# Kernel tuning notes

Measured on AMD Instinct MI355X. Metric: run time of the kernel, lower is better.

## Reference

```python
import jax, jax.numpy as jnp
import numpy as np

EPS = 1e-5

def _layernorm(x, gamma, beta):
    # normalize over last (channel) axis, per point
    mu = jnp.mean(x, axis=-1, keepdims=True)
    var = jnp.mean(jnp.square(x - mu), axis=-1, keepdims=True)
    return (x - mu) * jax.lax.rsqrt(var + EPS) * gamma + beta

def setup_inputs() -> dict:
    key = jax.random.key(0)
    ks = jax.random.split(key, 12)
    B, N, C, F = 32, 4096, 3, 1024
    points = jax.random.normal(ks[0], (B, N, C), dtype=jnp.float32)
    mask = jax.random.randint(ks[1], (B, 1, N), 0, 2, dtype=jnp.int32)
    s = 0.05
    return {
        "points": points,
        "mask": mask,
        "w1": jax.random.normal(ks[2], (128, C), dtype=jnp.float32) * s,      # conv1 (no bias)
        "g1": jnp.ones((128,), jnp.float32),                                   # norm1 gamma
        "be1": jnp.zeros((128,), jnp.float32),                                 # norm1 beta
        "w2": jax.random.normal(ks[3], (256, 128), dtype=jnp.float32) * s,     # conv2
        "b2": jax.random.normal(ks[4], (256,), dtype=jnp.float32) * s,
        "w3": jax.random.normal(ks[5], (512, 512), dtype=jnp.float32) * s,     # conv3 (no bias)
        "g2": jnp.ones((512,), jnp.float32),                                   # norm2 gamma
        "be2": jnp.zeros((512,), jnp.float32),                                 # norm2 beta
        "w4": jax.random.normal(ks[6], (F, 512), dtype=jnp.float32) * s,       # conv4
        "b4": jax.random.normal(ks[7], (F,), dtype=jnp.float32) * s,
    }

def reference(points, mask, w1, g1, be1, w2, b2, w3, g2, be2, w4, b4):
    # points: [B, N, C]; mask: [B, 1, N]
    vis = (mask[:, 0, :] != 0).astype(points.dtype)[..., None]  # [B, N, 1]
    # conv1 (1x1, no bias) as point-wise matmul
    h0 = jnp.einsum('bnc,kc->bnk', points, w1)                  # [B, N, 128]
    # masked LayerNorm: LN is per-point over channels, so compute densely and zero invisible points
    h1 = _layernorm(h0, g1, be1) * vis
    h2 = jax.nn.relu(h1)
    h3 = jnp.einsum('bnk,ok->bno', h2, w2) + b2                 # [B, N, 256]
    gmax = jnp.max(h3, axis=1, keepdims=True)                   # [B, 1, 256]
    dist = jnp.concatenate([jnp.broadcast_to(gmax, h3.shape), h3], axis=-1)  # [B, N, 512]
    h4 = jnp.einsum('bno,po->bnp', dist, w3)                    # [B, N, 512]
    h5 = _layernorm(h4, g2, be2) * vis
    h6 = jax.nn.relu(h5)
    h7 = jnp.einsum('bnp,fp->bnf', h6, w4) + b4                 # [B, N, F]
    return jnp.max(h7, axis=1)                                  # [B, F]
```

## Files before the change

### kernel.cpp

```cpp
#include <hip/hip_runtime.h>
#include <stdint.h>

#define LN_EPS 1e-5f

static __device__ __forceinline__ unsigned short f2bf_bits(float f) {
  union { float f; unsigned u; } v; v.f = f;
  unsigned r = v.u + 0x7FFFu + ((v.u >> 16) & 1u);
  return (unsigned short)(r >> 16);
}
static __device__ __forceinline__ float bf2f(unsigned short h) {
  union { unsigned u; float f; } v; v.u = ((unsigned)h) << 16;
  return v.f;
}

typedef __bf16 bf16x8 __attribute__((ext_vector_type(8)));
typedef float floatx4 __attribute__((ext_vector_type(4)));

typedef __attribute__((address_space(1))) unsigned int* gas_ptr;
typedef __attribute__((address_space(3))) unsigned int* las_ptr;
static __device__ __forceinline__ void async_cp16(const void* g, void* l) {
  __builtin_amdgcn_global_load_lds((gas_ptr)g, (las_ptr)l, 16, 0, 0);
}

__global__ __launch_bounds__(256) void perm_kernel(
    const int* __restrict__ mask, int* __restrict__ newrow, int* __restrict__ cnt) {
  const int b = blockIdx.x, t = threadIdx.x;
  const int base = b * 4096 + t * 16;
  int v[16]; int s = 0;
#pragma unroll
  for (int i = 0; i < 16; ++i) { v[i] = (mask[base + i] != 0); s += v[i]; }
  const int lane = t & 63, wv = t >> 6;
  int scan = s;
  for (int o = 1; o < 64; o <<= 1) { int x = __shfl_up(scan, o); if (lane >= o) scan += x; }
  __shared__ int wsum[4], woff[4], stotal;
  if (lane == 63) wsum[wv] = scan;
  __syncthreads();
  if (t == 0) { int a = 0; for (int k = 0; k < 4; ++k) { woff[k] = a; a += wsum[k]; } stotal = a; cnt[b] = a; }
  __syncthreads();
  const int excl = scan - s + woff[wv];
  const int total = stotal;
  int run = 0;
#pragma unroll
  for (int i = 0; i < 16; ++i) {
    const int pos = t * 16 + i;
    const int visBefore = excl + run;
    newrow[b * 4096 + pos] = v[i] ? visBefore : total + (pos - visBefore);
    run += v[i];
  }
}

__global__ __launch_bounds__(256) void conv1_ln_kernel(
    const float* __restrict__ points,
    const float* __restrict__ w1, const float* __restrict__ g1,
    const float* __restrict__ be1, unsigned short* __restrict__ h2,
    const int* __restrict__ newrow, const int* __restrict__ cnt,
    const float* __restrict__ w2, const float* __restrict__ b2,
    const float* __restrict__ w3, const float* __restrict__ w4,
    unsigned short* __restrict__ w2b, unsigned short* __restrict__ w4b,
    unsigned short* __restrict__ w23b, float* __restrict__ vecb,
    int* __restrict__ hdr, unsigned short* __restrict__ tl128,
    unsigned short* __restrict__ tl256) {
  if (blockIdx.x >= 32768) {
    const int bb = blockIdx.x - 32768;
    if (bb < 2176) {
      int idx = bb * 256 + threadIdx.x;
      if (idx < 32768) w2b[idx] = f2bf_bits(w2[idx]);
      else w4b[idx - 32768] = f2bf_bits(w4[idx - 32768]);
    } else if (bb < 2176 + 256) {
      const int tid = threadIdx.x;
      const int p = (bb - 2176) * 2 + (tid >> 7);
      const int c = tid & 127;
      const float* w3r = w3 + (size_t)p * 512 + 256;
      float s = 0.f;
      for (int k = 0; k < 256; ++k) s += w3r[k] * w2[k * 128 + c];
      w23b[p * 128 + c] = f2bf_bits(s);
      if (c == 0) {
        float vb = 0.f;
        for (int k = 0; k < 256; ++k) vb += w3r[k] * b2[k];
        vecb[p] = vb;
      }
    } else {
      const int lane = threadIdx.x;
      if (lane < 64) {
        const int c = (lane < 32) ? cnt[lane] : 0;
        const int n128 = (c + 127) >> 7;
        const int n256 = (c + 255) >> 8;
        int s128 = n128, s256 = n256;
        for (int o = 1; o < 64; o <<= 1) {
          int x = __shfl_up(s128, o); if (lane >= o) s128 += x;
          int y = __shfl_up(s256, o); if (lane >= o) s256 += y;
        }
        if (lane == 31) { hdr[0] = s128; hdr[1] = s256; }
        if (lane < 32) {
          const int e128 = s128 - n128, e256 = s256 - n256;
          for (int j = 0; j < n128; ++j) tl128[e128 + j] = (unsigned short)(lane * 32 + j);
          for (int j = 0; j < n256; ++j) tl256[e256 + j] = (unsigned short)(lane * 16 + j);
        }
      }
    }
    return;
  }
  const int lane = threadIdx.x & 63;
  const int wv = threadIdx.x >> 6;
  const size_t p = (size_t)blockIdx.x * 4 + wv;
  const int dest = newrow[p];
  const int cntb = cnt[p >> 12];
  const int ceilv = (cntb + 127) & ~127;
  if (dest >= ceilv) return;
  const bool vis = (dest < cntb);
  const float x0 = points[p * 3 + 0];
  const float x1 = points[p * 3 + 1];
  const float x2 = points[p * 3 + 2];
  const int c0 = lane * 2, c1 = c0 + 1;
  float h00 = w1[c0 * 3] * x0 + w1[c0 * 3 + 1] * x1 + w1[c0 * 3 + 2] * x2;
  float h01 = w1[c1 * 3] * x0 + w1[c1 * 3 + 1] * x1 + w1[c1 * 3 + 2] * x2;
  float s = h00 + h01;
  for (int o = 32; o; o >>= 1) s += __shfl_xor(s, o);
  const float mu = s * (1.f / 128.f);
  const float d0 = h00 - mu, d1 = h01 - mu;
  float q = d0 * d0 + d1 * d1;
  for (int o = 32; o; o >>= 1) q += __shfl_xor(q, o);
  const float rs = rsqrtf(q * (1.f / 128.f) + LN_EPS);
  const float y0 = vis ? fmaxf(d0 * rs * g1[c0] + be1[c0], 0.f) : 0.f;
  const float y1 = vis ? fmaxf(d1 * rs * g1[c1] + be1[c1], 0.f) : 0.f;
  union { unsigned u; unsigned short s2[2]; } pk;
  pk.s2[0] = f2bf_bits(y0);
  pk.s2[1] = f2bf_bits(y1);
  const size_t prow = (p & ~(size_t)4095) + (size_t)dest;
  ((unsigned*)h2)[prow * 64 + lane] = pk.u;
}

__global__ __launch_bounds__(256) void gemm23_fused(
    const unsigned short* __restrict__ A,
    const unsigned short* __restrict__ w2b, const unsigned short* __restrict__ w23b,
    unsigned short* __restrict__ h46, float* __restrict__ pg,
    const float* __restrict__ b2, const float* __restrict__ vecb,
    const int* __restrict__ hdr, const unsigned short* __restrict__ tl128) {
  __shared__ __align__(16) char smA[2][128 * 64];
  __shared__ __align__(16) char smB[2][128 * 64];
  __shared__ float lmax[2][128];

  const int nW = hdr[0] * 6;
  if (blockIdx.x >= nW) return;
  const int t6 = blockIdx.x / 6;
  const int colTile = blockIdx.x - t6 * 6;
  const int rowTile = tl128[t6];

  const int tid = threadIdx.x;
  const int lane = tid & 63;
  const int w = tid >> 6;
  const int wm = w >> 1, wn = w & 1;

  const bool isPG = (colTile < 2);
  const int colBase = isPG ? colTile * 128 : (colTile - 2) * 128;
  const size_t rowBase = (size_t)rowTile * 128;
  const unsigned short* Bw = isPG ? w2b : w23b;

  floatx4 acc[4][4];
  const floatx4 zero = {0.f, 0.f, 0.f, 0.f};
#pragma unroll
  for (int i = 0; i < 4; ++i)
#pragma unroll
    for (int j = 0; j < 4; ++j) acc[i][j] = zero;

  const int rSub = lane >> 2;
  const int cb16 = (lane & 3) * 16;
  const size_t Kb = 256;
  const char* gA = (const char*)A + (rowBase + (size_t)(w * 32 + rSub)) * Kb + cb16;
  const char* gB = (const char*)Bw + ((size_t)colBase + (size_t)(w * 32 + rSub)) * Kb + cb16;
  char* lA0 = smA[0] + w * 2048;
  char* lA1 = smA[1] + w * 2048;
  char* lB0 = smB[0] + w * 2048;
  char* lB1 = smB[1] + w * 2048;
  const size_t skip16 = 16 * Kb;

  const int fm = lane & 15, fq = lane >> 4;
  const int fOff = fm * 64 + fq * 16;
  const char* pa0 = smA[0] + wm * 64 * 64 + fOff;
  const char* pa1 = smA[1] + wm * 64 * 64 + fOff;
  const char* pb0 = smB[0] + wn * 64 * 64 + fOff;
  const char* pb1 = smB[1] + wn * 64 * 64 + fOff;

  for (int k0 = 0; k0 < 128; k0 += 64) {
    async_cp16(gA, lA0);
    async_cp16(gA + skip16, lA0 + 1024);
    async_cp16(gA + 64, lA1);
    async_cp16(gA + 64 + skip16, lA1 + 1024);
    async_cp16(gB, lB0);
    async_cp16(gB + skip16, lB0 + 1024);
    async_cp16(gB + 64, lB1);
    async_cp16(gB + 64 + skip16, lB1 + 1024);
    gA += 128; gB += 128;
    __syncthreads();
    bf16x8 af0[4], bg0[4], af1[4], bg1[4];
#pragma unroll
    for (int i = 0; i < 4; ++i) af0[i] = *(const bf16x8*)(pa0 + i * 16 * 64);
#pragma unroll
    for (int j = 0; j < 4; ++j) bg0[j] = *(const bf16x8*)(pb0 + j * 16 * 64);
#pragma unroll
    for (int i = 0; i < 4; ++i)
#pragma unroll
      for (int j = 0; j < 4; ++j)
        acc[i][j] = __builtin_amdgcn_mfma_f32_16x16x32_bf16(af0[i], bg0[j], acc[i][j], 0, 0, 0);
#pragma unroll
    for (int i = 0; i < 4; ++i) af1[i] = *(const bf16x8*)(pa1 + i * 16 * 64);
#pragma unroll
    for (int j = 0; j < 4; ++j) bg1[j] = *(const bf16x8*)(pb1 + j * 16 * 64);
#pragma unroll
    for (int i = 0; i < 4; ++i)
#pragma unroll
      for (int j = 0; j < 4; ++j)
        acc[i][j] = __builtin_amdgcn_mfma_f32_16x16x32_bf16(af1[i], bg1[j], acc[i][j], 0, 0, 0);
    __syncthreads();
  }

  if (isPG) {
    float m4[4] = {-1e30f, -1e30f, -1e30f, -1e30f};
#pragma unroll
    for (int j = 0; j < 4; ++j) {
      const float ex = b2[colBase + wn * 64 + j * 16 + fm];
#pragma unroll
      for (int i = 0; i < 4; ++i)
#pragma unroll
        for (int r = 0; r < 4; ++r) m4[j] = fmaxf(m4[j], acc[i][j][r] + ex);
      m4[j] = fmaxf(m4[j], __shfl_xor(m4[j], 16));
      m4[j] = fmaxf(m4[j], __shfl_xor(m4[j], 32));
    }
    const float sel = (fq == 0) ? m4[0] : (fq == 1) ? m4[1] : (fq == 2) ? m4[2] : m4[3];
    lmax[wm][wn * 64 + fq * 16 + fm] = sel;
    __syncthreads();
    if (tid < 128) {
      const float v = fmaxf(lmax[0][tid], lmax[1][tid]);
      pg[(size_t)rowTile * 256 + colBase + tid] = v;
    }
  } else {
#pragma unroll
    for (int j = 0; j < 4; ++j) {
      const int col = colBase + wn * 64 + j * 16 + fm;
      const float ex = vecb[col];
#pragma unroll
      for (int i = 0; i < 4; ++i) {
        const size_t row0 = rowBase + wm * 64 + i * 16 + fq * 4;
#pragma unroll
        for (int r = 0; r < 4; ++r) {
          h46[(row0 + r) * 512 + col] = f2bf_bits(acc[i][j][r] + ex);
        }
      }
    }
  }
}

#define G4_BAR() __builtin_amdgcn_s_barrier()
#define G4_LGKM0() asm volatile("s_waitcnt lgkmcnt(0)" ::: "memory")
#define G4_LGKM8() asm volatile("s_waitcnt lgkmcnt(8)" ::: "memory")
#define G4_VM2() asm volatile("s_waitcnt vmcnt(2)" ::: "memory")
#define G4_VM0() asm volatile("s_waitcnt vmcnt(0)" ::: "memory")
#define G4_PRIO1() __builtin_amdgcn_s_setprio(1)
#define G4_PRIO0() __builtin_amdgcn_s_setprio(0)

#define G4_STG(bufi, h4, kt) do { \
  const char* _s = (((h4) < 2) ? srcA : srcB) + (size_t)((h4) & 1) * (128 * 1024) + (size_t)(kt) * 128; \
  char* _d = stDst + (bufi) * 65536 + ((h4) >> 1) * 32768 + ((h4) & 1) * 16384; \
  async_cp16(_s, _d); \
  async_cp16(_s + 64 * 1024, _d + 8192); \
} while (0)

#define G4_LDA(bufi, mh) do { \
  const char* _p = rdA + (bufi) * 65536 + (mh) * 8192; \
  af[0][0] = *(const bf16x8*)(_p + c0);        af[0][1] = *(const bf16x8*)(_p + c1); \
  af[1][0] = *(const bf16x8*)(_p + 2048 + c0); af[1][1] = *(const bf16x8*)(_p + 2048 + c1); \
  af[2][0] = *(const bf16x8*)(_p + 4096 + c0); af[2][1] = *(const bf16x8*)(_p + 4096 + c1); \
  af[3][0] = *(const bf16x8*)(_p + 6144 + c0); af[3][1] = *(const bf16x8*)(_p + 6144 + c1); \
} while (0)

#define G4_LDB(bufi, nh, bgx) do { \
  const char* _p = rdB + (bufi) * 65536 + (nh) * 4096; \
  bgx[0][0] = *(const bf16x8*)(_p + c0);        bgx[0][1] = *(const bf16x8*)(_p + c1); \
  bgx[1][0] = *(const bf16x8*)(_p + 2048 + c0); bgx[1][1] = *(const bf16x8*)(_p + 2048 + c1); \
} while (0)

#define G4_QUAD(mh, nh, bgx) do { \
  _Pragma("unroll") \
  for (int _m = 0; _m < 4; ++_m) { \
    _Pragma("unroll") \
    for (int _n = 0; _n < 2; ++_n) { \
      acc[(mh) * 4 + _m][(nh) * 2 + _n] = __builtin_amdgcn_mfma_f32_16x16x32_bf16( \
          af[_m][0], bgx[_n][0], acc[(mh) * 4 + _m][(nh) * 2 + _n], 0, 0, 0); \
      acc[(mh) * 4 + _m][(nh) * 2 + _n] = __builtin_amdgcn_mfma_f32_16x16x32_bf16( \
          af[_m][1], bgx[_n][1], acc[(mh) * 4 + _m][(nh) * 2 + _n], 0, 0, 0); \
    } \
  } \
} while (0)

__global__ __launch_bounds__(512, 2) void gemm4_8ph(
    const unsigned short* __restrict__ A, const unsigned short* __restrict__ Bw,
    float* __restrict__ outp2, const int* __restrict__ hdr,
    const unsigned short* __restrict__ tl256) {
  extern __shared__ char sm[];

  const int nW = hdr[1] * 4;
  if (blockIdx.x >= nW) return;
  const int rowTile = tl256[blockIdx.x >> 2];
  const int colTile = blockIdx.x & 3;

  const int tid = threadIdx.x;
  const int lane = tid & 63;
  const int w = tid >> 6;
  const int wm = w >> 2, wn = w & 3;

  const size_t rowBase = (size_t)rowTile * 256;
  const int colBase = colTile * 256;

  const int rr = tid >> 3;
  const int csw = ((tid & 7) ^ (rr & 7)) << 4;
  const char* srcA = (const char*)A + (rowBase + (size_t)rr) * 1024 + csw;
  const char* srcB = (const char*)Bw + ((size_t)colBase + (size_t)rr) * 1024 + csw;
  char* stDst = sm + w * 1024;

  const int fr = lane & 15, fq = lane >> 4;
  const int c0 = (fq * 16) ^ ((lane & 7) << 4);
  const int c1 = ((fq * 16) | 64) ^ ((lane & 7) << 4);
  const char* rdA = sm + (wm * 128 + fr) * 128;
  const char* rdB = sm + 32768 + (wn * 64 + fr) * 128;

  floatx4 acc[8][4];
  const floatx4 zero = {0.f, 0.f, 0.f, 0.f};
#pragma unroll
  for (int i = 0; i < 8; ++i)
#pragma unroll
    for (int j = 0; j < 4; ++j) acc[i][j] = zero;

  bf16x8 af[4][2], bg0[2][2], bg1[2][2];

  G4_STG(0, 0, 0); G4_STG(0, 1, 0); G4_STG(0, 2, 0); G4_STG(0, 3, 0);
  G4_STG(1, 0, 1);
  G4_VM2(); G4_BAR();

  for (int it = 0; it < 3; ++it) {
    const int tO = 2 * it + 1, tE2 = 2 * it + 2, tO2 = 2 * it + 3;
    G4_LDA(0, 0); G4_LDB(0, 0, bg0); G4_STG(1, 1, tO); G4_LGKM8(); G4_BAR(); G4_LGKM0();
    G4_PRIO1(); G4_QUAD(0, 0, bg0); G4_PRIO0(); G4_BAR();
    G4_LDB(0, 1, bg1); G4_STG(1, 2, tO); G4_BAR(); G4_LGKM0();
    G4_PRIO1(); G4_QUAD(0, 1, bg1); G4_PRIO0(); G4_BAR();
    G4_LDA(0, 1); G4_STG(1, 3, tO); G4_BAR(); G4_LGKM0();
    G4_PRIO1(); G4_QUAD(1, 1, bg1); G4_PRIO0(); G4_BAR();
    G4_STG(0, 0, tE2); G4_VM2(); G4_BAR();
    G4_PRIO1(); G4_QUAD(1, 0, bg0); G4_PRIO0(); G4_BAR();
    G4_LDA(1, 0); G4_LDB(1, 0, bg0); G4_STG(0, 1, tE2); G4_LGKM8(); G4_BAR(); G4_LGKM0();
    G4_PRIO1(); G4_QUAD(0, 0, bg0); G4_PRIO0(); G4_BAR();
    G4_LDB(1, 1, bg1); G4_STG(0, 2, tE2); G4_BAR(); G4_LGKM0();
    G4_PRIO1(); G4_QUAD(0, 1, bg1); G4_PRIO0(); G4_BAR();
    G4_LDA(1, 1); G4_STG(0, 3, tE2); G4_BAR(); G4_LGKM0();
    G4_PRIO1(); G4_QUAD(1, 1, bg1); G4_PRIO0(); G4_BAR();
    G4_STG(1, 0, tO2); G4_VM2(); G4_BAR();
    G4_PRIO1(); G4_QUAD(1, 0, bg0); G4_PRIO0(); G4_BAR();
  }

  G4_LDA(0, 0); G4_LDB(0, 0, bg0); G4_STG(1, 1, 7); G4_LGKM8(); G4_BAR(); G4_LGKM0();
  G4_PRIO1(); G4_QUAD(0, 0, bg0); G4_PRIO0(); G4_BAR();
  G4_LDB(0, 1, bg1); G4_STG(1, 2, 7); G4_BAR(); G4_LGKM0();
  G4_PRIO1(); G4_QUAD(0, 1, bg1); G4_PRIO0(); G4_BAR();
  G4_LDA(0, 1); G4_STG(1, 3, 7); G4_BAR(); G4_LGKM0();
  G4_PRIO1(); G4_QUAD(1, 1, bg1); G4_PRIO0(); G4_BAR();
  G4_VM0(); G4_BAR();
  G4_PRIO1(); G4_QUAD(1, 0, bg0); G4_PRIO0(); G4_BAR();
  G4_LDA(1, 0); G4_LDB(1, 0, bg0); G4_BAR(); G4_LGKM0();
  G4_PRIO1(); G4_QUAD(0, 0, bg0); G4_PRIO0(); G4_BAR();
  G4_LDB(1, 1, bg1); G4_BAR(); G4_LGKM0();
  G4_PRIO1(); G4_QUAD(0, 1, bg1); G4_PRIO0(); G4_BAR();
  G4_LDA(1, 1); G4_BAR(); G4_LGKM0();
  G4_PRIO1(); G4_QUAD(1, 1, bg1); G4_PRIO0(); G4_BAR();
  G4_PRIO1(); G4_QUAD(1, 0, bg0); G4_PRIO0(); G4_BAR();

  float* smf = (float*)sm;
  float mv[4];
#pragma unroll
  for (int nj = 0; nj < 4; ++nj) {
    float m = -1e30f;
#pragma unroll
    for (int mi = 0; mi < 8; ++mi)
#pragma unroll
      for (int r = 0; r < 4; ++r) m = fmaxf(m, acc[mi][nj][r]);
    m = fmaxf(m, __shfl_xor(m, 16));
    m = fmaxf(m, __shfl_xor(m, 32));
    mv[nj] = m;
  }
  const float sel = (fq == 0) ? mv[0] : (fq == 1) ? mv[1] : (fq == 2) ? mv[2] : mv[3];
  smf[wm * 256 + wn * 64 + fq * 16 + fr] = sel;
  __syncthreads();
  if (tid < 256) {
    outp2[(size_t)rowTile * 1024 + colBase + tid] = fmaxf(smf[tid], smf[256 + tid]);
  }
}

__global__ __launch_bounds__(256) void gmax_cvec_kernel(
    const float* __restrict__ pg, const float* __restrict__ w3,
    float* __restrict__ cvec, const int* __restrict__ cnt,
    const float* __restrict__ b2) {
  __shared__ float gm[256];
  const int b = blockIdx.x >> 2, quarter = blockIdx.x & 3;
  const int t = threadIdx.x;
  const int c = cnt[b];
  const int nt = (c + 127) >> 7;
  float m = (c < 4096) ? b2[t] : -1e30f;
  for (int s = 0; s < nt; ++s) m = fmaxf(m, pg[((size_t)b * 32 + s) * 256 + t]);
  gm[t] = m;
  __syncthreads();
  const int lane = t & 63, wv = t >> 6;
  const float g0 = gm[lane * 4 + 0];
  const float g1 = gm[lane * 4 + 1];
  const float g2v = gm[lane * 4 + 2];
  const float g3 = gm[lane * 4 + 3];
  for (int pp = 0; pp < 32; ++pp) {
    const int p = quarter * 128 + wv * 32 + pp;
    const float4 wr = *(const float4*)(w3 + (size_t)p * 512 + lane * 4);
    float s = wr.x * g0 + wr.y * g1 + wr.z * g2v + wr.w * g3;
    for (int o = 32; o; o >>= 1) s += __shfl_xor(s, o);
    if (lane == 0) cvec[b * 512 + p] = s;
  }
}

__global__ __launch_bounds__(256) void ln2_kernel(
    unsigned short* __restrict__ h46, const int* __restrict__ cnt,
    const float* __restrict__ cvec,
    const float* __restrict__ g2, const float* __restrict__ be2,
    const int* __restrict__ hdr, const unsigned short* __restrict__ tl256) {
  const int nW = hdr[1] * 64;
  if (blockIdx.x >= nW) return;
  const int rowTile = tl256[blockIdx.x >> 6];
  const int lane = threadIdx.x & 63;
  const int wv = threadIdx.x >> 6;
  const size_t p = (size_t)rowTile * 256 + ((blockIdx.x & 63) * 4 + wv);
  const int b = rowTile >> 4;
  const int cb = cnt[b];
  const int pin = (int)(p & 4095);
  unsigned short* row = h46 + p * 512;
  const int c0 = lane * 8;
  if (pin >= cb) {
    const uint4 z = {0, 0, 0, 0};
    *(uint4*)(row + c0) = z;
    return;
  }
  union { uint4 v; unsigned short s[8]; } in;
  in.v = *(const uint4*)(row + c0);
  float cv[8];
  *(float4*)(cv) = *(const float4*)(cvec + b * 512 + c0);
  *(float4*)(cv + 4) = *(const float4*)(cvec + b * 512 + c0 + 4);
  float f[8];
  float s = 0.f;
#pragma unroll
  for (int k = 0; k < 8; ++k) { f[k] = bf2f(in.s[k]) + cv[k]; s += f[k]; }
  for (int o = 32; o; o >>= 1) s += __shfl_xor(s, o);
  const float mu = s * (1.f / 512.f);
  float q = 0.f;
#pragma unroll
  for (int k = 0; k < 8; ++k) { const float d = f[k] - mu; q += d * d; }
  for (int o = 32; o; o >>= 1) q += __shfl_xor(q, o);
  const float rs = rsqrtf(q * (1.f / 512.f) + LN_EPS);
  union { uint4 v; unsigned short s[8]; } outv;
#pragma unroll
  for (int k = 0; k < 8; ++k) {
    const float y = fmaxf((f[k] - mu) * rs * g2[c0 + k] + be2[c0 + k], 0.f);
    outv.s[k] = f2bf_bits(y);
  }
  *(uint4*)(row + c0) = outv.v;
}

__global__ __launch_bounds__(256) void final_kernel(
    const float* __restrict__ pmax, const float* __restrict__ b4,
    float* __restrict__ out, const int* __restrict__ cnt) {
  const int idx = blockIdx.x * 256 + threadIdx.x;
  const int b = idx >> 10, f = idx & 1023;
  const int c = cnt[b];
  const int nt = (c + 255) >> 8;
  float m = (c < 4096) ? 0.f : -1e30f;
  for (int r = 0; r < nt; ++r) m = fmaxf(m, pmax[((size_t)(b * 16 + r)) * 1024 + f]);
  out[idx] = m + b4[f];
}

extern "C" void kernel_launch(void* const* d_in, const int* in_sizes, int n_in,
                              void* d_out, int out_size, void* d_ws, size_t ws_size,
                              hipStream_t stream) {
  const float* points = (const float*)d_in[0];
  const int* mask = (const int*)d_in[1];
  const float* w1 = (const float*)d_in[2];
  const float* g1 = (const float*)d_in[3];
  const float* be1 = (const float*)d_in[4];
  const float* w2 = (const float*)d_in[5];
  const float* b2 = (const float*)d_in[6];
  const float* w3 = (const float*)d_in[7];
  const float* g2 = (const float*)d_in[8];
  const float* be2 = (const float*)d_in[9];
  const float* w4 = (const float*)d_in[10];
  const float* b4 = (const float*)d_in[11];
  float* out = (float*)d_out;
  char* ws = (char*)d_ws;

  const size_t OFF_H46 = 0;
  const size_t OFF_H2 = 134217728;
  const size_t OFF_W2B = OFF_H2 + 33554432;
  const size_t OFF_W4B = OFF_W2B + 65536;
  const size_t OFF_W23B = OFF_W4B + 1048576;
  const size_t OFF_VECB = OFF_W23B + 131072;
  const size_t OFF_PG = OFF_VECB + 2048;
  const size_t OFF_CVEC = OFF_PG + 1048576;
  const size_t OFF_PMAX = OFF_CVEC + 65536;
  const size_t OFF_CNT = OFF_PMAX + 4194304;
  const size_t OFF_NEWROW = OFF_CNT + 4096;
  const size_t OFF_HDR = OFF_NEWROW + 524288;
  const size_t OFF_TL128 = OFF_HDR + 64;
  const size_t OFF_TL256 = OFF_TL128 + 2048;

  unsigned short* h2 = (unsigned short*)(ws + OFF_H2);
  unsigned short* h46 = (unsigned short*)(ws + OFF_H46);
  unsigned short* w2b = (unsigned short*)(ws + OFF_W2B);
  unsigned short* w4b = (unsigned short*)(ws + OFF_W4B);
  unsigned short* w23b = (unsigned short*)(ws + OFF_W23B);
  float* vecb = (float*)(ws + OFF_VECB);
  float* pg = (float*)(ws + OFF_PG);
  float* cvecp = (float*)(ws + OFF_CVEC);
  float* pmaxp = (float*)(ws + OFF_PMAX);
  int* cntp = (int*)(ws + OFF_CNT);
  int* newrow = (int*)(ws + OFF_NEWROW);
  int* hdr = (int*)(ws + OFF_HDR);
  unsigned short* tl128 = (unsigned short*)(ws + OFF_TL128);
  unsigned short* tl256 = (unsigned short*)(ws + OFF_TL256);

  static bool s_attr_done = false;
  if (!s_attr_done) {
    hipFuncSetAttribute((const void*)gemm4_8ph,
                        hipFuncAttributeMaxDynamicSharedMemorySize, 131072);
    s_attr_done = true;
  }

  perm_kernel<<<32, 256, 0, stream>>>(mask, newrow, cntp);
  conv1_ln_kernel<<<32768 + 2176 + 256 + 1, 256, 0, stream>>>(
      points, w1, g1, be1, h2, newrow, cntp, w2, b2, w3, w4, w2b, w4b, w23b, vecb,
      hdr, tl128, tl256);
  gemm23_fused<<<6144, 256, 0, stream>>>(h2, w2b, w23b, h46, pg, b2, vecb, hdr, tl128);
  gmax_cvec_kernel<<<128, 256, 0, stream>>>(pg, w3, cvecp, cntp, b2);
  ln2_kernel<<<32768, 256, 0, stream>>>(h46, cntp, cvecp, g2, be2, hdr, tl256);
  gemm4_8ph<<<2048, 512, 131072, stream>>>(h46, w4b, pmaxp, hdr, tl256);
  final_kernel<<<128, 256, 0, stream>>>(pmaxp, b4, out, cntp);
}
```

Baseline: 284.6 us.

## Make gemm4 persistent with XCD-aware work split and prefetch next tile

The final GEMM becomes a persistent kernel with 256 blocks. Each block strides through a contiguous chunk of work items assigned per XCD and issues the first global-to-LDS stages of the next tile before the epilogue max-reduction of the current one. Reduction scratch moves to a separate LDS region beyond the 128KB staging buffers so the prefetch does not clobber it. gemm23 also remaps block indices so consecutive work items land on the same XCD, aiming for better L2 reuse. The risks are load imbalance from the fixed chunking and lower occupancy, since LDS use now exceeds 128KB.

```diff
diff --git a/kernel.cpp b/kernel.cpp
--- a/kernel.cpp
+++ b/kernel.cpp
@@ -141,9 +141,12 @@
   __shared__ float lmax[2][128];
 
   const int nW = hdr[0] * 6;
-  if (blockIdx.x >= nW) return;
-  const int t6 = blockIdx.x / 6;
-  const int colTile = blockIdx.x - t6 * 6;
+  const int cw = (nW + 7) >> 3;
+  const int slot = blockIdx.x >> 3;
+  const int wI = (blockIdx.x & 7) * cw + slot;
+  if (slot >= cw || wI >= nW) return;
+  const int t6 = wI / 6;
+  const int colTile = wI - t6 * 6;
   const int rowTile = tl128[t6];
 
   const int tid = threadIdx.x;
@@ -299,22 +302,22 @@
   extern __shared__ char sm[];
 
   const int nW = hdr[1] * 4;
-  if (blockIdx.x >= nW) return;
-  const int rowTile = tl256[blockIdx.x >> 2];
-  const int colTile = blockIdx.x & 3;
+  const int cw = (nW + 7) >> 3;
+  const int xcd = blockIdx.x & 7;
+  const int cuid = blockIdx.x >> 3;
+  const int wLo = xcd * cw;
+  const int wHiRaw = wLo + cw;
+  const int wHi = (wHiRaw < nW) ? wHiRaw : nW;
+  int w_item = wLo + cuid;
+  if (w_item >= wHi) return;
 
   const int tid = threadIdx.x;
   const int lane = tid & 63;
   const int w = tid >> 6;
   const int wm = w >> 2, wn = w & 3;
 
-  const size_t rowBase = (size_t)rowTile * 256;
-  const int colBase = colTile * 256;
-
   const int rr = tid >> 3;
   const int csw = ((tid & 7) ^ (rr & 7)) << 4;
-  const char* srcA = (const char*)A + (rowBase + (size_t)rr) * 1024 + csw;
-  const char* srcB = (const char*)Bw + ((size_t)colBase + (size_t)rr) * 1024 + csw;
   char* stDst = sm + w * 1024;
 
   const int fr = lane & 15, fq = lane >> 4;
@@ -322,74 +325,94 @@
   const int c1 = ((fq * 16) | 64) ^ ((lane & 7) << 4);
   const char* rdA = sm + (wm * 128 + fr) * 128;
   const char* rdB = sm + 32768 + (wn * 64 + fr) * 128;
+  float* smf = (float*)(sm + 131072);
 
   floatx4 acc[8][4];
   const floatx4 zero = {0.f, 0.f, 0.f, 0.f};
-#pragma unroll
-  for (int i = 0; i < 8; ++i)
-#pragma unroll
-    for (int j = 0; j < 4; ++j) acc[i][j] = zero;
-
   bf16x8 af[4][2], bg0[2][2], bg1[2][2];
 
+  int rowTile = tl256[w_item >> 2];
+  int colBase = (w_item & 3) * 256;
+  const char* srcA = (const char*)A + ((size_t)rowTile * 256 + (size_t)rr) * 1024 + csw;
+  const char* srcB = (const char*)Bw + ((size_t)colBase + (size_t)rr) * 1024 + csw;
   G4_STG(0, 0, 0); G4_STG(0, 1, 0); G4_STG(0, 2, 0); G4_STG(0, 3, 0);
   G4_STG(1, 0, 1);
-  G4_VM2(); G4_BAR();
-
-  for (int it = 0; it < 3; ++it) {
-    const int tO = 2 * it + 1, tE2 = 2 * it + 2, tO2 = 2 * it + 3;
-    G4_LDA(0, 0); G4_LDB(0, 0, bg0); G4_STG(1, 1, tO); G4_LGKM8(); G4_BAR(); G4_LGKM0();
+
+  for (;;) {
+    G4_VM2(); G4_BAR();
+#pragma unroll
+    for (int i = 0; i < 8; ++i)
+#pragma unroll
+      for (int j = 0; j < 4; ++j) acc[i][j] = zero;
+
+    for (int it = 0; it < 3; ++it) {
+      const int tO = 2 * it + 1, tE2 = 2 * it + 2, tO2 = 2 * it + 3;
+      G4_LDA(0, 0); G4_LDB(0, 0, bg0); G4_STG(1, 1, tO); G4_LGKM8(); G4_BAR(); G4_LGKM0();
+      G4_PRIO1(); G4_QUAD(0, 0, bg0); G4_PRIO0(); G4_BAR();
+      G4_LDB(0, 1, bg1); G4_STG(1, 2, tO); G4_BAR(); G4_LGKM0();
+      G4_PRIO1(); G4_QUAD(0, 1, bg1); G4_PRIO0(); G4_BAR();
+      G4_LDA(0, 1); G4_STG(1, 3, tO); G4_BAR(); G4_LGKM0();
+      G4_PRIO1(); G4_QUAD(1, 1, bg1); G4_PRIO0(); G4_BAR();
+      G4_STG(0, 0, tE2); G4_VM2(); G4_BAR();
+      G4_PRIO1(); G4_QUAD(1, 0, bg0); G4_PRIO0(); G4_BAR();
+      G4_LDA(1, 0); G4_LDB(1, 0, bg0); G4_STG(0, 1, tE2); G4_LGKM8(); G4_BAR(); G4_LGKM0();
+      G4_PRIO1(); G4_QUAD(0, 0, bg0); G4_PRIO0(); G4_BAR();
+      G4_LDB(1, 1, bg1); G4_STG(0, 2, tE2); G4_BAR(); G4_LGKM0();
+      G4_PRIO1(); G4_QUAD(0, 1, bg1); G4_PRIO0(); G4_BAR();
+      G4_LDA(1, 1); G4_STG(0, 3, tE2); G4_BAR(); G4_LGKM0();
+      G4_PRIO1(); G4_QUAD(1, 1, bg1); G4_PRIO0(); G4_BAR();
+      G4_STG(1, 0, tO2); G4_VM2(); G4_BAR();
+      G4_PRIO1(); G4_QUAD(1, 0, bg0); G4_PRIO0(); G4_BAR();
+    }
+
+    G4_LDA(0, 0); G4_LDB(0, 0, bg0); G4_STG(1, 1, 7); G4_LGKM8(); G4_BAR(); G4_LGKM0();
     G4_PRIO1(); G4_QUAD(0, 0, bg0); G4_PRIO0(); G4_BAR();
-    G4_LDB(0, 1, bg1); G4_STG(1, 2, tO); G4_BAR(); G4_LGKM0();
+    G4_LDB(0, 1, bg1); G4_STG(1, 2, 7); G4_BAR(); G4_LGKM0();
     G4_PRIO1(); G4_QUAD(0, 1, bg1); G4_PRIO0(); G4_BAR();
-    G4_LDA(0, 1); G4_STG(1, 3, tO); G4_BAR(); G4_LGKM0();
+    G4_LDA(0, 1); G4_STG(1, 3, 7); G4_BAR(); G4_LGKM0();
     G4_PRIO1(); G4_QUAD(1, 1, bg1); G4_PRIO0(); G4_BAR();
-    G4_STG(0, 0, tE2); G4_VM2(); G4_BAR();
+    G4_VM0(); G4_BAR();
     G4_PRIO1(); G4_QUAD(1, 0, bg0); G4_PRIO0(); G4_BAR();
-    G4_LDA(1, 0); G4_LDB(1, 0, bg0); G4_STG(0, 1, tE2); G4_LGKM8(); G4_BAR(); G4_LGKM0();
+    G4_LDA(1, 0); G4_LDB(1, 0, bg0); G4_BAR(); G4_LGKM0();
     G4_PRIO1(); G4_QUAD(0, 0, bg0); G4_PRIO0(); G4_BAR();
-    G4_LDB(1, 1, bg1); G4_STG(0, 2, tE2); G4_BAR(); G4_LGKM0();
+    G4_LDB(1, 1, bg1); G4_BAR(); G4_LGKM0();
     G4_PRIO1(); G4_QUAD(0, 1, bg1); G4_PRIO0(); G4_BAR();
-    G4_LDA(1, 1); G4_STG(0, 3, tE2); G4_BAR(); G4_LGKM0();
+    G4_LDA(1, 1); G4_BAR(); G4_LGKM0();
     G4_PRIO1(); G4_QUAD(1, 1, bg1); G4_PRIO0(); G4_BAR();
-    G4_STG(1, 0, tO2); G4_VM2(); G4_BAR();
     G4_PRIO1(); G4_QUAD(1, 0, bg0); G4_PRIO0(); G4_BAR();
-  }
-
-  G4_LDA(0, 0); G4_LDB(0, 0, bg0); G4_STG(1, 1, 7); G4_LGKM8(); G4_BAR(); G4_LGKM0();
-  G4_PRIO1(); G4_QUAD(0, 0, bg0); G4_PRIO0(); G4_BAR();
-  G4_LDB(0, 1, bg1); G4_STG(1, 2, 7); G4_BAR(); G4_LGKM0();
-  G4_PRIO1(); G4_QUAD(0, 1, bg1); G4_PRIO0(); G4_BAR();
-  G4_LDA(0, 1); G4_STG(1, 3, 7); G4_BAR(); G4_LGKM0();
-  G4_PRIO1(); G4_QUAD(1, 1, bg1); G4_PRIO0(); G4_BAR();
-  G4_VM0(); G4_BAR();
-  G4_PRIO1(); G4_QUAD(1, 0, bg0); G4_PRIO0(); G4_BAR();
-  G4_LDA(1, 0); G4_LDB(1, 0, bg0); G4_BAR(); G4_LGKM0();
-  G4_PRIO1(); G4_QUAD(0, 0, bg0); G4_PRIO0(); G4_BAR();
-  G4_LDB(1, 1, bg1); G4_BAR(); G4_LGKM0();
-  G4_PRIO1(); G4_QUAD(0, 1, bg1); G4_PRIO0(); G4_BAR();
-  G4_LDA(1, 1); G4_BAR(); G4_LGKM0();
-  G4_PRIO1(); G4_QUAD(1, 1, bg1); G4_PRIO0(); G4_BAR();
-  G4_PRIO1(); G4_QUAD(1, 0, bg0); G4_PRIO0(); G4_BAR();
-
-  float* smf = (float*)sm;
-  float mv[4];
-#pragma unroll
-  for (int nj = 0; nj < 4; ++nj) {
-    float m = -1e30f;
-#pragma unroll
-    for (int mi = 0; mi < 8; ++mi)
-#pragma unroll
-      for (int r = 0; r < 4; ++r) m = fmaxf(m, acc[mi][nj][r]);
-    m = fmaxf(m, __shfl_xor(m, 16));
-    m = fmaxf(m, __shfl_xor(m, 32));
-    mv[nj] = m;
-  }
-  const float sel = (fq == 0) ? mv[0] : (fq == 1) ? mv[1] : (fq == 2) ? mv[2] : mv[3];
-  smf[wm * 256 + wn * 64 + fq * 16 + fr] = sel;
-  __syncthreads();
-  if (tid < 256) {
-    outp2[(size_t)rowTile * 1024 + colBase + tid] = fmaxf(smf[tid], smf[256 + tid]);
+
+    const int curRow = rowTile, curCol = colBase;
+    const int w_next = w_item + 32;
+    const bool more = (w_next < wHi);
+    if (more) {
+      rowTile = tl256[w_next >> 2];
+      colBase = (w_next & 3) * 256;
+      srcA = (const char*)A + ((size_t)rowTile * 256 + (size_t)rr) * 1024 + csw;
+      srcB = (const char*)Bw + ((size_t)colBase + (size_t)rr) * 1024 + csw;
+      G4_STG(0, 0, 0); G4_STG(0, 1, 0); G4_STG(0, 2, 0); G4_STG(0, 3, 0);
+      G4_STG(1, 0, 1);
+    }
+
+    float mv[4];
+#pragma unroll
+    for (int nj = 0; nj < 4; ++nj) {
+      float m = -1e30f;
+#pragma unroll
+      for (int mi = 0; mi < 8; ++mi)
+#pragma unroll
+        for (int r = 0; r < 4; ++r) m = fmaxf(m, acc[mi][nj][r]);
+      m = fmaxf(m, __shfl_xor(m, 16));
+      m = fmaxf(m, __shfl_xor(m, 32));
+      mv[nj] = m;
+    }
+    const float sel = (fq == 0) ? mv[0] : (fq == 1) ? mv[1] : (fq == 2) ? mv[2] : mv[3];
+    smf[wm * 256 + wn * 64 + fq * 16 + fr] = sel;
+    G4_LGKM0(); G4_BAR();
+    if (tid < 256) {
+      outp2[(size_t)curRow * 1024 + curCol + tid] = fmaxf(smf[tid], smf[256 + tid]);
+    }
+    if (!more) break;
+    w_item = w_next;
   }
 }
 
@@ -529,7 +552,7 @@
   static bool s_attr_done = false;
   if (!s_attr_done) {
     hipFuncSetAttribute((const void*)gemm4_8ph,
-                        hipFuncAttributeMaxDynamicSharedMemorySize, 131072);
+                        hipFuncAttributeMaxDynamicSharedMemorySize, 133120);
     s_attr_done = true;
   }
 
@@ -540,6 +563,6 @@
   gemm23_fused<<<6144, 256, 0, stream>>>(h2, w2b, w23b, h46, pg, b2, vecb, hdr, tl128);
   gmax_cvec_kernel<<<128, 256, 0, stream>>>(pg, w3, cvecp, cntp, b2);
   ln2_kernel<<<32768, 256, 0, stream>>>(h46, cntp, cvecp, g2, be2, hdr, tl256);
-  gemm4_8ph<<<2048, 512, 131072, stream>>>(h46, w4b, pmaxp, hdr, tl256);
+  gemm4_8ph<<<256, 512, 133120, stream>>>(h46, w4b, pmaxp, hdr, tl256);
   final_kernel<<<128, 256, 0, stream>>>(pmaxp, b4, out, cntp);
 }
```

Measured after the change: 297.6 us. 1.05x slower.
